# Kernel optimization log

Hardware: AMD Instinct MI355X
Metric: run time of the kernel (lower is better)

Reference implementation:

```python
import jax, jax.numpy as jnp
import numpy as np

MAX_ITER = 20   # init kwarg max_iter
EPS = 1e-10     # init kwarg epsilon


def setup_inputs() -> dict:
    key = jax.random.key(0)
    k1, k2, k3 = jax.random.split(key, 3)
    B, M, N = 256, 512, 512
    s = jax.random.uniform(k1, (B, M, N), dtype=jnp.float32)
    nrows = jax.random.randint(k2, (B,), 1, M + 1, dtype=jnp.int32)
    ncols = jax.random.randint(k3, (B,), 1, N + 1, dtype=jnp.int32)
    return {"s": s, "nrows": nrows, "ncols": ncols}


def _sinkhorn(s, nrows, ncols):
    # Masked Sinkhorn-Knopp: alternately normalize columns (even iters) and
    # rows (odd iters) over each batch element's valid [0:nrows, 0:ncols] block.
    # Entries outside the valid block are zeroed each iteration (matches the
    # original, which only writes 1/sum into the valid slice of `tmp`).
    B, M, N = s.shape
    rm = (jnp.arange(M)[None, :] < nrows[:, None]).astype(s.dtype)   # [B, M]
    cm = (jnp.arange(N)[None, :] < ncols[:, None]).astype(s.dtype)   # [B, N]
    block = rm[:, :, None] * cm[:, None, :]                           # [B, M, N]
    s = s + EPS
    for i in range(MAX_ITER):
        if i % 2 == 1:
            # row sums over valid columns -> normalize rows, denom [B, M, 1]
            denom = jnp.sum(s * cm[:, None, :], axis=2, keepdims=True)
        else:
            # column sums over valid rows -> normalize columns, denom [B, 1, N]
            denom = jnp.sum(s * rm[:, :, None], axis=1, keepdims=True)
        denom = jnp.where(denom > 0, denom, jnp.ones_like(denom))  # avoid 0/0 outside block
        s = jnp.where(block > 0, s / denom, jnp.zeros_like(s))
    return s


def reference(s, nrows, ncols):
    return _sinkhorn(s, nrows, ncols)
```

## Files before the change

### kernel.cpp

```cpp
#include <hip/hip_runtime.h>

#define SEPS 1e-10f
typedef unsigned int uu;

__device__ __forceinline__ uu bfpack2(float f0, float f1) {
    uu u0 = __float_as_uint(f0 + SEPS);
    uu u1 = __float_as_uint(f1 + SEPS);
    u0 += 0x7FFFu + ((u0 >> 16) & 1u);
    u1 += 0x7FFFu + ((u1 >> 16) & 1u);
    return (u0 >> 16) | (u1 & 0xFFFF0000u);
}
__device__ __forceinline__ float blo(uu w){ return __uint_as_float(w << 16); }
__device__ __forceinline__ float bhi(uu w){ return __uint_as_float(w & 0xFFFF0000u); }
__device__ __forceinline__ float grcp(float x){ return (x > 0.f) ? __builtin_amdgcn_rcpf(x) : 1.f; }

__global__
__attribute__((amdgpu_flat_work_group_size(1024, 1024)))
void sinkhorn_kernel(const float* __restrict__ s, const int* __restrict__ nrows,
                     const int* __restrict__ ncols, float* __restrict__ out)
{
    __shared__ __align__(16) float cpart[16][512];
    __shared__ float sh_u[512];
    __shared__ float sh_v[512];

    const int b   = blockIdx.x;
    const int tid = threadIdx.x;
    const int wv  = tid >> 6;
    const int wl  = tid & 63;
    const int nr  = nrows[b];
    const int nc  = ncols[b];

    float* ob = out + ((size_t)b << 18);
    uu*    W0 = (uu*)ob + 131072;
    const float4* sb4 = (const float4*)(s + ((size_t)b << 18));
    float4* ob4 = (float4*)ob;

    #pragma unroll 4
    for (int it = 0; it < 64; ++it) {
        const int f = it * 1024 + tid;
        const int r = f >> 7, p = f & 127;
        float4 w = sb4[f];
        const int rem = nc - 4 * p;
        const uu mA = (rem >= 2) ? 0xFFFFFFFFu : ((rem == 1) ? 0x0000FFFFu : 0u);
        const uu mB = (rem >= 4) ? 0xFFFFFFFFu : ((rem == 3) ? 0x0000FFFFu : 0u);
        const uu rm = (r < nr) ? 0xFFFFFFFFu : 0u;
        *(uint2*)(W0 + r * 256 + 2 * p) = make_uint2(bfpack2(w.x, w.y) & mA & rm,
                                                     bfpack2(w.z, w.w) & mB & rm);
    }
    __syncthreads();

    const uu* wp = W0 + wl * 4;

    {
        float ce0=0,co0=0,ce1=0,co1=0,ce2=0,co2=0,ce3=0,co3=0;
        #pragma unroll 4
        for (int g = 0; g < 32; ++g) {
            const int i = (g << 4) + wv;
            uint4 wq = *(const uint4*)(wp + i * 256);
            ce0 += blo(wq.x); co0 += bhi(wq.x);
            ce1 += blo(wq.y); co1 += bhi(wq.y);
            ce2 += blo(wq.z); co2 += bhi(wq.z);
            ce3 += blo(wq.w); co3 += bhi(wq.w);
        }
        float* cw = &cpart[wv][wl * 8];
        cw[0]=ce0; cw[1]=co0; cw[2]=ce1; cw[3]=co1;
        cw[4]=ce2; cw[5]=co2; cw[6]=ce3; cw[7]=co3;
    }
    __syncthreads();
    if (tid < 512) {
        float sum = 0.f;
        #pragma unroll
        for (int w = 0; w < 16; ++w) sum += cpart[w][tid];
        sh_v[tid] = grcp(sum);
    }
    __syncthreads();

    #pragma unroll 1
    for (int sw = 0; sw < 9; ++sw) {
        const float4 va = *(const float4*)&sh_v[wl * 8];
        const float4 vb = *(const float4*)&sh_v[wl * 8 + 4];
        float ce0=0,co0=0,ce1=0,co1=0,ce2=0,co2=0,ce3=0,co3=0;
        #pragma unroll 4
        for (int g = 0; g < 32; ++g) {
            const int i = (g << 4) + wv;
            uint4 wq = *(const uint4*)(wp + i * 256);
            float p = blo(wq.x)*va.x + bhi(wq.x)*va.y
                    + blo(wq.y)*va.z + bhi(wq.y)*va.w
                    + blo(wq.z)*vb.x + bhi(wq.z)*vb.y
                    + blo(wq.w)*vb.z + bhi(wq.w)*vb.w;
            p += __shfl_xor(p, 1);  p += __shfl_xor(p, 2);  p += __shfl_xor(p, 4);
            p += __shfl_xor(p, 8);  p += __shfl_xor(p, 16); p += __shfl_xor(p, 32);
            const float u = grcp(p);
            ce0 += blo(wq.x)*u; co0 += bhi(wq.x)*u;
            ce1 += blo(wq.y)*u; co1 += bhi(wq.y)*u;
            ce2 += blo(wq.z)*u; co2 += bhi(wq.z)*u;
            ce3 += blo(wq.w)*u; co3 += bhi(wq.w)*u;
        }
        float* cw = &cpart[wv][wl * 8];
        cw[0]=ce0; cw[1]=co0; cw[2]=ce1; cw[3]=co1;
        cw[4]=ce2; cw[5]=co2; cw[6]=ce3; cw[7]=co3;
        __syncthreads();
        if (tid < 512) {
            float sum = 0.f;
            #pragma unroll
            for (int w = 0; w < 16; ++w) sum += cpart[w][tid];
            sh_v[tid] = grcp(sum);
        }
        __syncthreads();
    }

    {
        const float4 va = *(const float4*)&sh_v[wl * 8];
        const float4 vb = *(const float4*)&sh_v[wl * 8 + 4];
        #pragma unroll 4
        for (int g = 0; g < 32; ++g) {
            const int i = (g << 4) + wv;
            uint4 wq = *(const uint4*)(wp + i * 256);
            float p = blo(wq.x)*va.x + bhi(wq.x)*va.y
                    + blo(wq.y)*va.z + bhi(wq.y)*va.w
                    + blo(wq.z)*vb.x + bhi(wq.z)*vb.y
                    + blo(wq.w)*vb.z + bhi(wq.w)*vb.w;
            p += __shfl_xor(p, 1);  p += __shfl_xor(p, 2);  p += __shfl_xor(p, 4);
            p += __shfl_xor(p, 8);  p += __shfl_xor(p, 16); p += __shfl_xor(p, 32);
            if (wl == 0) sh_u[i] = grcp(p);
        }
    }
    __syncthreads();

    uu* stg = (uu*)cpart;
    {
        uint4* d4 = (uint4*)stg;
        const uint4* s4 = (const uint4*)(W0 + 480 * 256);
        d4[tid]        = s4[tid];
        d4[tid + 1024] = s4[tid + 1024];
    }
    __syncthreads();
    {
        const int p  = tid & 127;
        const int rs = tid >> 7;
        const float4 vv = make_float4(sh_v[4*p], sh_v[4*p+1], sh_v[4*p+2], sh_v[4*p+3]);
        #pragma unroll 1
        for (int m = 0; m < 16; ++m) {
            if (m >= 8) __syncthreads();
            #pragma unroll
            for (int it = 0; it < 4; ++it) {
                const int i = (m << 5) + (it << 3) + rs;
                const uint2 tw = (m == 15)
                    ? *(const uint2*)(stg + (i - 480) * 256 + 2 * p)
                    : *(const uint2*)(W0 + i * 256 + 2 * p);
                const float uk = sh_u[i];
                float4 o;
                o.x = blo(tw.x) * uk * vv.x;
                o.y = bhi(tw.x) * uk * vv.y;
                o.z = blo(tw.y) * uk * vv.z;
                o.w = bhi(tw.y) * uk * vv.w;
                ob4[i * 128 + p] = o;
            }
        }
    }
}

extern "C" void kernel_launch(void* const* d_in, const int* in_sizes, int n_in,
                              void* d_out, int out_size, void* d_ws, size_t ws_size,
                              hipStream_t stream) {
    const float* s     = (const float*)d_in[0];
    const int*   nrows = (const int*)d_in[1];
    const int*   ncols = (const int*)d_in[2];
    float*       out   = (float*)d_out;
    const int B = in_sizes[1];
    sinkhorn_kernel<<<dim3(B), dim3(1024), 0, stream>>>(s, nrows, ncols, out);
}
```

Baseline: 670.9 us.

## Fuse initial column sums into load pass and cache scratch rows in registers/LDS

The first column-sum pass now runs during the fp32-to-bf16 packing loop, which saves one full re-read of the scratch matrix. The loop mapping changes so that each thread owns a fixed column group across rows. Rows 0–127 of each thread's slice are kept in registers and rows 128–239 are copied into a new ~112KB LDS buffer. The Sinkhorn sweeps therefore fetch only the remaining rows from global/L2 memory. In exchange, register and LDS use rise sharply, which pushes LDS close to the per-CU limit and keeps occupancy at one block per CU.

Measured after the change: 1.388 ms. +106.8%, slower.

```diff
diff --git a/kernel.cpp b/kernel.cpp
--- a/kernel.cpp
+++ b/kernel.cpp
@@ -19,6 +19,7 @@
 void sinkhorn_kernel(const float* __restrict__ s, const int* __restrict__ nrows,
                      const int* __restrict__ ncols, float* __restrict__ out)
 {
+    __shared__ __align__(16) uu    w_lds[112 * 256];
     __shared__ __align__(16) float cpart[16][512];
     __shared__ float sh_u[512];
     __shared__ float sh_v[512];
@@ -35,66 +36,75 @@
     const float4* sb4 = (const float4*)(s + ((size_t)b << 18));
     float4* ob4 = (float4*)ob;
 
-    #pragma unroll 4
-    for (int it = 0; it < 64; ++it) {
-        const int f = it * 1024 + tid;
-        const int r = f >> 7, p = f & 127;
-        float4 w = sb4[f];
+    {
+        const int p  = tid & 127;
+        const int t8 = tid >> 7;
         const int rem = nc - 4 * p;
         const uu mA = (rem >= 2) ? 0xFFFFFFFFu : ((rem == 1) ? 0x0000FFFFu : 0u);
         const uu mB = (rem >= 4) ? 0xFFFFFFFFu : ((rem == 3) ? 0x0000FFFFu : 0u);
-        const uu rm = (r < nr) ? 0xFFFFFFFFu : 0u;
-        *(uint2*)(W0 + r * 256 + 2 * p) = make_uint2(bfpack2(w.x, w.y) & mA & rm,
-                                                     bfpack2(w.z, w.w) & mB & rm);
+        float cA = 0.f, cB = 0.f, cC = 0.f, cD = 0.f;
+        #pragma unroll 4
+        for (int k = 0; k < 64; ++k) {
+            const int r = (k << 3) + t8;
+            float4 w = sb4[r * 128 + p];
+            const uu rm = (r < nr) ? 0xFFFFFFFFu : 0u;
+            const uu px = bfpack2(w.x, w.y) & mA & rm;
+            const uu py = bfpack2(w.z, w.w) & mB & rm;
+            *(uint2*)(W0 + r * 256 + 2 * p) = make_uint2(px, py);
+            cA += blo(px); cB += bhi(px); cC += blo(py); cD += bhi(py);
+        }
+        *(float4*)&cpart[t8][4 * p] = make_float4(cA, cB, cC, cD);
     }
     __syncthreads();
 
+    {
+        const uint4* s4 = (const uint4*)(W0 + 128 * 256);
+        uint4* d4 = (uint4*)w_lds;
+        #pragma unroll
+        for (int it = 0; it < 7; ++it)
+            d4[it * 1024 + tid] = s4[it * 1024 + tid];
+    }
     const uu* wp = W0 + wl * 4;
+    uint4 R0 = *(const uint4*)(wp + (  0 + wv) * 256);
+    uint4 R1 = *(const uint4*)(wp + ( 16 + wv) * 256);
+    uint4 R2 = *(const uint4*)(wp + ( 32 + wv) * 256);
+    uint4 R3 = *(const uint4*)(wp + ( 48 + wv) * 256);
+    uint4 R4 = *(const uint4*)(wp + ( 64 + wv) * 256);
+    uint4 R5 = *(const uint4*)(wp + ( 80 + wv) * 256);
+    uint4 R6 = *(const uint4*)(wp + ( 96 + wv) * 256);
+    uint4 R7 = *(const uint4*)(wp + (112 + wv) * 256);
 
-    {
-        float ce0=0,co0=0,ce1=0,co1=0,ce2=0,co2=0,ce3=0,co3=0;
-        #pragma unroll 4
-        for (int g = 0; g < 32; ++g) {
-            const int i = (g << 4) + wv;
-            uint4 wq = *(const uint4*)(wp + i * 256);
-            ce0 += blo(wq.x); co0 += bhi(wq.x);
-            ce1 += blo(wq.y); co1 += bhi(wq.y);
-            ce2 += blo(wq.z); co2 += bhi(wq.z);
-            ce3 += blo(wq.w); co3 += bhi(wq.w);
-        }
-        float* cw = &cpart[wv][wl * 8];
-        cw[0]=ce0; cw[1]=co0; cw[2]=ce1; cw[3]=co1;
-        cw[4]=ce2; cw[5]=co2; cw[6]=ce3; cw[7]=co3;
-    }
-    __syncthreads();
     if (tid < 512) {
-        float sum = 0.f;
-        #pragma unroll
-        for (int w = 0; w < 16; ++w) sum += cpart[w][tid];
+        float sum = cpart[0][tid] + cpart[1][tid] + cpart[2][tid] + cpart[3][tid]
+                  + cpart[4][tid] + cpart[5][tid] + cpart[6][tid] + cpart[7][tid];
         sh_v[tid] = grcp(sum);
     }
     __syncthreads();
+
+#define ROWF(wq) { \
+    float p_ = blo(wq.x)*va.x + bhi(wq.x)*va.y + blo(wq.y)*va.z + bhi(wq.y)*va.w \
+             + blo(wq.z)*vb.x + bhi(wq.z)*vb.y + blo(wq.w)*vb.z + bhi(wq.w)*vb.w; \
+    p_ += __shfl_xor(p_, 1);  p_ += __shfl_xor(p_, 2);  p_ += __shfl_xor(p_, 4); \
+    p_ += __shfl_xor(p_, 8);  p_ += __shfl_xor(p_, 16); p_ += __shfl_xor(p_, 32); \
+    const float u_ = grcp(p_); \
+    ce0 += blo(wq.x)*u_; co0 += bhi(wq.x)*u_; ce1 += blo(wq.y)*u_; co1 += bhi(wq.y)*u_; \
+    ce2 += blo(wq.z)*u_; co2 += bhi(wq.z)*u_; ce3 += blo(wq.w)*u_; co3 += bhi(wq.w)*u_; }
 
     #pragma unroll 1
     for (int sw = 0; sw < 9; ++sw) {
         const float4 va = *(const float4*)&sh_v[wl * 8];
         const float4 vb = *(const float4*)&sh_v[wl * 8 + 4];
         float ce0=0,co0=0,ce1=0,co1=0,ce2=0,co2=0,ce3=0,co3=0;
+        ROWF(R0) ROWF(R1) ROWF(R2) ROWF(R3) ROWF(R4) ROWF(R5) ROWF(R6) ROWF(R7)
+        #pragma unroll
+        for (int g = 8; g < 15; ++g) {
+            uint4 wq = *(const uint4*)(w_lds + (16 * g + wv - 128) * 256 + wl * 4);
+            ROWF(wq)
+        }
         #pragma unroll 4
-        for (int g = 0; g < 32; ++g) {
-            const int i = (g << 4) + wv;
-            uint4 wq = *(const uint4*)(wp + i * 256);
-            float p = blo(wq.x)*va.x + bhi(wq.x)*va.y
-                    + blo(wq.y)*va.z + bhi(wq.y)*va.w
-                    + blo(wq.z)*vb.x + bhi(wq.z)*vb.y
-                    + blo(wq.w)*vb.z + bhi(wq.w)*vb.w;
-            p += __shfl_xor(p, 1);  p += __shfl_xor(p, 2);  p += __shfl_xor(p, 4);
-            p += __shfl_xor(p, 8);  p += __shfl_xor(p, 16); p += __shfl_xor(p, 32);
-            const float u = grcp(p);
-            ce0 += blo(wq.x)*u; co0 += bhi(wq.x)*u;
-            ce1 += blo(wq.y)*u; co1 += bhi(wq.y)*u;
-            ce2 += blo(wq.z)*u; co2 += bhi(wq.z)*u;
-            ce3 += blo(wq.w)*u; co3 += bhi(wq.w)*u;
+        for (int g = 15; g < 32; ++g) {
+            uint4 wq = *(const uint4*)(wp + (16 * g + wv) * 256);
+            ROWF(wq)
         }
         float* cw = &cpart[wv][wl * 8];
         cw[0]=ce0; cw[1]=co0; cw[2]=ce1; cw[3]=co1;
@@ -109,20 +119,26 @@
         __syncthreads();
     }
 
+#define FINROW(wq, i) { \
+    float p_ = blo(wq.x)*va.x + bhi(wq.x)*va.y + blo(wq.y)*va.z + bhi(wq.y)*va.w \
+             + blo(wq.z)*vb.x + bhi(wq.z)*vb.y + blo(wq.w)*vb.z + bhi(wq.w)*vb.w; \
+    p_ += __shfl_xor(p_, 1);  p_ += __shfl_xor(p_, 2);  p_ += __shfl_xor(p_, 4); \
+    p_ += __shfl_xor(p_, 8);  p_ += __shfl_xor(p_, 16); p_ += __shfl_xor(p_, 32); \
+    if (wl == 0) sh_u[i] = grcp(p_); }
     {
         const float4 va = *(const float4*)&sh_v[wl * 8];
         const float4 vb = *(const float4*)&sh_v[wl * 8 + 4];
+        FINROW(R0,   0 + wv) FINROW(R1,  16 + wv) FINROW(R2,  32 + wv) FINROW(R3,  48 + wv)
+        FINROW(R4,  64 + wv) FINROW(R5,  80 + wv) FINROW(R6,  96 + wv) FINROW(R7, 112 + wv)
+        #pragma unroll
+        for (int g = 8; g < 15; ++g) {
+            uint4 wq = *(const uint4*)(w_lds + (16 * g + wv - 128) * 256 + wl * 4);
+            FINROW(wq, 16 * g + wv)
+        }
         #pragma unroll 4
-        for (int g = 0; g < 32; ++g) {
-            const int i = (g << 4) + wv;
-            uint4 wq = *(const uint4*)(wp + i * 256);
-            float p = blo(wq.x)*va.x + bhi(wq.x)*va.y
-                    + blo(wq.y)*va.z + bhi(wq.y)*va.w
-                    + blo(wq.z)*vb.x + bhi(wq.z)*vb.y
-                    + blo(wq.w)*vb.z + bhi(wq.w)*vb.w;
-            p += __shfl_xor(p, 1);  p += __shfl_xor(p, 2);  p += __shfl_xor(p, 4);
-            p += __shfl_xor(p, 8);  p += __shfl_xor(p, 16); p += __shfl_xor(p, 32);
-            if (wl == 0) sh_u[i] = grcp(p);
+        for (int g = 15; g < 32; ++g) {
+            uint4 wq = *(const uint4*)(wp + (16 * g + wv) * 256);
+            FINROW(wq, 16 * g + wv)
         }
     }
     __syncthreads();
@@ -136,9 +152,9 @@
     }
     __syncthreads();
     {
-        const int p  = tid & 127;
+        const int ep = tid & 127;
         const int rs = tid >> 7;
-        const float4 vv = make_float4(sh_v[4*p], sh_v[4*p+1], sh_v[4*p+2], sh_v[4*p+3]);
+        const float4 vv = make_float4(sh_v[4*ep], sh_v[4*ep+1], sh_v[4*ep+2], sh_v[4*ep+3]);
         #pragma unroll 1
         for (int m = 0; m < 16; ++m) {
             if (m >= 8) __syncthreads();
@@ -146,15 +162,15 @@
             for (int it = 0; it < 4; ++it) {
                 const int i = (m << 5) + (it << 3) + rs;
                 const uint2 tw = (m == 15)
-                    ? *(const uint2*)(stg + (i - 480) * 256 + 2 * p)
-                    : *(const uint2*)(W0 + i * 256 + 2 * p);
+                    ? *(const uint2*)(stg + (i - 480) * 256 + 2 * ep)
+                    : *(const uint2*)(W0 + i * 256 + 2 * ep);
                 const float uk = sh_u[i];
                 float4 o;
                 o.x = blo(tw.x) * uk * vv.x;
                 o.y = bhi(tw.x) * uk * vv.y;
                 o.z = blo(tw.y) * uk * vv.z;
                 o.w = bhi(tw.y) * uk * vv.w;
-                ob4[i * 128 + p] = o;
+                ob4[i * 128 + ep] = o;
             }
         }
     }
```
